# Optimization experiments

Hardware: AMD Instinct MI355X
Metric: run time of the kernel (lower is better)

Reference implementation:

```python
import jax, jax.numpy as jnp
import numpy as np

N_NODES = 50000


def gcn_conv(x, W, b, src, dst, n_nodes):
    """PyG GCNConv: x' = D^-1/2 (A+I) D^-1/2 (x W) + b (symmetric norm, self-loops)."""
    h = x @ W  # [N, out]
    loop = jnp.arange(n_nodes, dtype=src.dtype)
    src_f = jnp.concatenate([src, loop])
    dst_f = jnp.concatenate([dst, loop])
    ones = jnp.ones(src_f.shape[0], dtype=h.dtype)
    deg = jax.ops.segment_sum(ones, dst_f, num_segments=n_nodes)
    dinv = jnp.where(deg > 0, jax.lax.rsqrt(deg), 0.0)
    norm = dinv[src_f] * dinv[dst_f]  # [E+N]
    msg = h[src_f] * norm[:, None]    # irregular gather over edges
    out = jax.ops.segment_sum(msg, dst_f, num_segments=n_nodes)
    return out + b


def setup_inputs() -> dict:
    key = jax.random.key(0)
    ks = jax.random.split(key, 9)
    d_in, d_h = 128, 128
    x = jax.random.normal(ks[0], (N_NODES, d_in), dtype=jnp.float32)
    edge_index = jax.random.randint(ks[1], (2, 800000), 0, N_NODES, dtype=jnp.int64)
    glorot = lambda k, fi, fo: jax.random.normal(k, (fi, fo), dtype=jnp.float32) * jnp.sqrt(2.0 / (fi + fo))
    return {
        "x": x,
        "edge_index": edge_index,
        "W1": glorot(ks[2], d_in, d_h), "b1": jnp.zeros((d_h,), jnp.float32),
        "W2": glorot(ks[3], d_h, d_h), "b2": jnp.zeros((d_h,), jnp.float32),
        "W3": glorot(ks[4], d_h, d_h), "b3": jnp.zeros((d_h,), jnp.float32),
    }


def reference(x, edge_index, W1, b1, W2, b2, W3, b3):
    src, dst = edge_index[0], edge_index[1]
    n = x.shape[0]
    h = jax.nn.relu(gcn_conv(x, W1, b1, src, dst, n))
    h = jax.nn.relu(gcn_conv(h, W2, b2, src, dst, n))
    h = gcn_conv(h, W3, b3, src, dst, n)
    return h
```

## Files before the change

kernel.cpp:

```cpp
#include <hip/hip_runtime.h>

#define N_NODES 50000
#define N_EDGES 800000
#define DIM 128
#define MAXDEG 80
#define EDGE_BLOCKS ((N_EDGES + 255) / 256)
#define WT_BLOCKS 192
#define GEMM_BLOCKS ((N_NODES + 127) / 128)

typedef unsigned int u32;
typedef short bf16x8 __attribute__((ext_vector_type(8)));
typedef float f32x4 __attribute__((ext_vector_type(4)));

static inline size_t alignUp(size_t x) { return (x + 255) & ~size_t(255); }

__device__ inline unsigned short f2bf(float f) {
    union { float f; u32 u; } v; v.f = f;
    u32 r = v.u + 0x7fffu + ((v.u >> 16) & 1u);
    return (unsigned short)(r >> 16);
}
__device__ inline float bf_lo(u32 u) { return __uint_as_float(u << 16); }
__device__ inline float bf_hi(u32 u) { return __uint_as_float(u & 0xffff0000u); }

__global__ __launch_bounds__(256) void prep_kernel(const float* __restrict__ W1,
                                                   const float* __restrict__ W2,
                                                   const float* __restrict__ W3,
                                                   unsigned short* __restrict__ Wt,
                                                   const int* __restrict__ src,
                                                   const int* __restrict__ dst,
                                                   int* __restrict__ cursor,
                                                   int* __restrict__ csr) {
    int bid = blockIdx.x;
    if (bid < WT_BLOCKS) {
        int m = bid >> 6;
        int e = (bid & 63) * 256 + threadIdx.x;
        int n = e >> 7, k = e & 127;
        const float* W = (m == 0) ? W1 : (m == 1) ? W2 : W3;
        Wt[m * DIM * DIM + n * DIM + k] = f2bf(W[(size_t)k * DIM + n]);
        return;
    }
    int i = (bid - WT_BLOCKS) * 256 + threadIdx.x;
    if (i < N_EDGES) {
        int d = dst[i];
        int pos = atomicAdd(&cursor[d], 1);
        if (pos < MAXDEG) csr[d * MAXDEG + pos] = src[i];
    }
}

#define LDSTRIDE 40
__global__ __launch_bounds__(256) void gemm_mfma_kernel(const float* __restrict__ x,
                                                        const unsigned short* __restrict__ Wt,
                                                        unsigned short* __restrict__ hb,
                                                        int n_rows) {
    __shared__ unsigned short As[128 * LDSTRIDE];
    __shared__ unsigned short Bs[128 * LDSTRIDE];
    const int tid = threadIdx.x;
    const int wave = tid >> 6;
    const int lane = tid & 63;
    const int quad = lane >> 4;
    const int l16 = lane & 15;
    const int row0 = blockIdx.x * 128;

    f32x4 acc[2][8];
#pragma unroll
    for (int mt = 0; mt < 2; mt++)
#pragma unroll
        for (int nt = 0; nt < 8; nt++) acc[mt][nt] = (f32x4){0.f, 0.f, 0.f, 0.f};

    for (int k0 = 0; k0 < DIM; k0 += 32) {
#pragma unroll
        for (int p = 0; p < 4; p++) {
            int r = p * 32 + (tid >> 3);
            int kq = (tid & 7) * 4;
            int gr = row0 + r;
            float4 v = make_float4(0.f, 0.f, 0.f, 0.f);
            if (gr < n_rows) v = *(const float4*)&x[(size_t)gr * DIM + k0 + kq];
            u32 lo = (u32)f2bf(v.x) | ((u32)f2bf(v.y) << 16);
            u32 hi = (u32)f2bf(v.z) | ((u32)f2bf(v.w) << 16);
            *(uint2*)&As[r * LDSTRIDE + kq] = make_uint2(lo, hi);
        }
#pragma unroll
        for (int p = 0; p < 2; p++) {
            int nn = p * 64 + (tid >> 2);
            int kk = (tid & 3) * 8;
            *(uint4*)&Bs[nn * LDSTRIDE + kk] = *(const uint4*)&Wt[nn * DIM + k0 + kk];
        }
        __syncthreads();
        const int m0 = wave * 32;
        bf16x8 a0 = *(const bf16x8*)&As[(m0 + l16) * LDSTRIDE + quad * 8];
        bf16x8 a1 = *(const bf16x8*)&As[(m0 + 16 + l16) * LDSTRIDE + quad * 8];
#pragma unroll
        for (int nt = 0; nt < 8; nt++) {
            bf16x8 b = *(const bf16x8*)&Bs[(nt * 16 + l16) * LDSTRIDE + quad * 8];
            acc[0][nt] = __builtin_amdgcn_mfma_f32_16x16x32_bf16(a0, b, acc[0][nt], 0, 0, 0);
            acc[1][nt] = __builtin_amdgcn_mfma_f32_16x16x32_bf16(a1, b, acc[1][nt], 0, 0, 0);
        }
        __syncthreads();
    }
    const int m0 = wave * 32;
#pragma unroll
    for (int mt = 0; mt < 2; mt++) {
#pragma unroll
        for (int reg = 0; reg < 4; reg++) {
            int gr = row0 + m0 + mt * 16 + quad * 4 + reg;
            if (gr < n_rows) {
#pragma unroll
                for (int nt = 0; nt < 8; nt++)
                    hb[(size_t)gr * DIM + nt * 16 + l16] = f2bf(acc[mt][nt][reg]);
            }
        }
    }
}

__device__ inline void accum8(float acc[8], uint4 r, float w) {
    acc[0] += w * bf_lo(r.x); acc[1] += w * bf_hi(r.x);
    acc[2] += w * bf_lo(r.y); acc[3] += w * bf_hi(r.y);
    acc[4] += w * bf_lo(r.z); acc[5] += w * bf_hi(r.z);
    acc[6] += w * bf_lo(r.w); acc[7] += w * bf_hi(r.w);
}

__global__ __launch_bounds__(256) void agg_kernel(const uint4* __restrict__ hb,
                                                  const int* __restrict__ cnt,
                                                  const int* __restrict__ csr,
                                                  const float4* __restrict__ bias4,
                                                  float* __restrict__ out, int relu) {
    const int wave = threadIdx.x >> 6;
    const int lane = threadIdx.x & 63;
    const int node = blockIdx.x * 4 + wave;
    const int g = lane >> 4;
    const int l16 = lane & 15;

    const int deg = cnt[node];
    const float di = rsqrtf((float)(deg + 1));
    const int m_total = min(deg, MAXDEG);
    const size_t start = (size_t)node * MAXDEG;

    float acc[8];
#pragma unroll
    for (int i = 0; i < 8; i++) acc[i] = 0.f;

    for (int base = 0; base < m_total; base += 64) {
        int m = min(64, m_total - base);
        int e = 0; float w = 0.f;
        if (lane < m) {
            e = csr[start + base + lane];
            w = rsqrtf((float)(cnt[e] + 1));
        }
        int j4 = 0;
        for (; j4 + 8 <= m; j4 += 8) {
            int j0 = j4 + g, j1 = j4 + 4 + g;
            int s0 = __shfl(e, j0, 64);  float w0 = __shfl(w, j0, 64);
            int s1 = __shfl(e, j1, 64);  float w1 = __shfl(w, j1, 64);
            uint4 r0 = hb[(size_t)s0 * 16 + l16];
            uint4 r1 = hb[(size_t)s1 * 16 + l16];
            accum8(acc, r0, w0);
            accum8(acc, r1, w1);
        }
        for (; j4 < m; j4 += 4) {
            int j = j4 + g;
            int jj = (j < m) ? j : 0;
            int s0 = __shfl(e, jj, 64);  float w0 = __shfl(w, jj, 64);
            if (j < m) {
                uint4 r0 = hb[(size_t)s0 * 16 + l16];
                accum8(acc, r0, w0);
            }
        }
    }
    if (g == 0) {
        uint4 r = hb[(size_t)node * 16 + l16];
        accum8(acc, r, di);
    }
#pragma unroll
    for (int i = 0; i < 8; i++) {
        acc[i] += __shfl_xor(acc[i], 16, 64);
        acc[i] += __shfl_xor(acc[i], 32, 64);
    }
    if (g == 0) {
        float4 b0 = bias4[l16 * 2], b1 = bias4[l16 * 2 + 1];
        float4 r0 = make_float4(di * acc[0] + b0.x, di * acc[1] + b0.y,
                                di * acc[2] + b0.z, di * acc[3] + b0.w);
        float4 r1 = make_float4(di * acc[4] + b1.x, di * acc[5] + b1.y,
                                di * acc[6] + b1.z, di * acc[7] + b1.w);
        if (relu) {
            r0.x = fmaxf(r0.x, 0.f); r0.y = fmaxf(r0.y, 0.f);
            r0.z = fmaxf(r0.z, 0.f); r0.w = fmaxf(r0.w, 0.f);
            r1.x = fmaxf(r1.x, 0.f); r1.y = fmaxf(r1.y, 0.f);
            r1.z = fmaxf(r1.z, 0.f); r1.w = fmaxf(r1.w, 0.f);
        }
        float4* o = (float4*)(out + (size_t)node * DIM);
        o[l16 * 2] = r0;
        o[l16 * 2 + 1] = r1;
    }
}


extern "C" void kernel_launch(void* const* d_in, const int* in_sizes, int n_in,
                              void* d_out, int out_size, void* d_ws, size_t ws_size,
                              hipStream_t stream) {
    const float* x  = (const float*)d_in[0];
    const int* ei   = (const int*)d_in[1];
    const float* W1 = (const float*)d_in[2];
    const float* b1 = (const float*)d_in[3];
    const float* W2 = (const float*)d_in[4];
    const float* b2 = (const float*)d_in[5];
    const float* W3 = (const float*)d_in[6];
    const float* b3 = (const float*)d_in[7];
    const int* src = ei;
    const int* dst = ei + N_EDGES;
    float* out = (float*)d_out;

    char* w = (char*)d_ws;
    int* cursor = (int*)w; w += alignUp((size_t)N_NODES * 4);
    int* csr    = (int*)w; w += alignUp((size_t)N_NODES * MAXDEG * 4);
    unsigned short* wt = (unsigned short*)w; w += alignUp((size_t)3 * DIM * DIM * 2);
    unsigned short* hbuf = (unsigned short*)w; w += alignUp((size_t)N_NODES * DIM * 2);
    float* fbuf = (float*)w; w += alignUp((size_t)N_NODES * DIM * 4);

    hipMemsetAsync(cursor, 0, (size_t)N_NODES * 4, stream);

    int ablocks = N_NODES / 4;

    prep_kernel<<<WT_BLOCKS + EDGE_BLOCKS, 256, 0, stream>>>(W1, W2, W3, wt, src, dst,
                                                             cursor, csr);

    gemm_mfma_kernel<<<GEMM_BLOCKS, 256, 0, stream>>>(x, wt, hbuf, N_NODES);
    agg_kernel<<<ablocks, 256, 0, stream>>>((const uint4*)hbuf, cursor, csr,
                                            (const float4*)b1, fbuf, 1);

    gemm_mfma_kernel<<<GEMM_BLOCKS, 256, 0, stream>>>(fbuf, wt + DIM * DIM, hbuf, N_NODES);
    agg_kernel<<<ablocks, 256, 0, stream>>>((const uint4*)hbuf, cursor, csr,
                                            (const float4*)b2, fbuf, 1);

    gemm_mfma_kernel<<<GEMM_BLOCKS, 256, 0, stream>>>(fbuf, wt + 2 * DIM * DIM, hbuf, N_NODES);
    agg_kernel<<<ablocks, 256, 0, stream>>>((const uint4*)hbuf, cursor, csr,
                                            (const float4*)b3, out, 0);
}
```

Before: 284.2 us.

## Build compact CSR with prefix-scan offsets, 16-bit indices, precomputed dinv

After: 317.0 us. +11.5%, slower.

```diff
diff --git a/kernel.cpp b/kernel.cpp
--- a/kernel.cpp
+++ b/kernel.cpp
@@ -3,10 +3,10 @@
 #define N_NODES 50000
 #define N_EDGES 800000
 #define DIM 128
-#define MAXDEG 80
 #define EDGE_BLOCKS ((N_EDGES + 255) / 256)
 #define WT_BLOCKS 192
 #define GEMM_BLOCKS ((N_NODES + 127) / 128)
+#define SCAN_BLOCKS ((N_NODES + 255) / 256)
 
 typedef unsigned int u32;
 typedef short bf16x8 __attribute__((ext_vector_type(8)));
@@ -26,10 +26,8 @@
                                                    const float* __restrict__ W2,
                                                    const float* __restrict__ W3,
                                                    unsigned short* __restrict__ Wt,
-                                                   const int* __restrict__ src,
                                                    const int* __restrict__ dst,
-                                                   int* __restrict__ cursor,
-                                                   int* __restrict__ csr) {
+                                                   int* __restrict__ cnt) {
     int bid = blockIdx.x;
     if (bid < WT_BLOCKS) {
         int m = bid >> 6;
@@ -40,10 +38,32 @@
         return;
     }
     int i = (bid - WT_BLOCKS) * 256 + threadIdx.x;
-    if (i < N_EDGES) {
-        int d = dst[i];
-        int pos = atomicAdd(&cursor[d], 1);
-        if (pos < MAXDEG) csr[d * MAXDEG + pos] = src[i];
+    if (i < N_EDGES) atomicAdd(&cnt[dst[i]], 1);
+}
+
+__global__ __launch_bounds__(256) void offsets_kernel(const int* __restrict__ cnt,
+                                                      int* __restrict__ total,
+                                                      int* __restrict__ base,
+                                                      int* __restrict__ cur,
+                                                      float* __restrict__ dinv) {
+    int i = blockIdx.x * 256 + threadIdx.x;
+    int lane = threadIdx.x & 63;
+    int c = (i < N_NODES) ? cnt[i] : 0;
+    int v = c;
+#pragma unroll
+    for (int off = 1; off < 64; off <<= 1) {
+        int u = __shfl_up(v, off, 64);
+        if (lane >= off) v += u;
+    }
+    int wsum = __shfl(v, 63, 64);
+    int wbase = 0;
+    if (lane == 63) wbase = atomicAdd(total, wsum);
+    wbase = __shfl(wbase, 63, 64);
+    if (i < N_NODES) {
+        int b = wbase + v - c;
+        base[i] = b;
+        cur[i]  = b;
+        dinv[i] = rsqrtf((float)(c + 1));
     }
 }
 
@@ -51,7 +71,20 @@
 __global__ __launch_bounds__(256) void gemm_mfma_kernel(const float* __restrict__ x,
                                                         const unsigned short* __restrict__ Wt,
                                                         unsigned short* __restrict__ hb,
-                                                        int n_rows) {
+                                                        int n_rows,
+                                                        const int* __restrict__ src,
+                                                        const int* __restrict__ dst,
+                                                        int* __restrict__ cur,
+                                                        unsigned short* __restrict__ csr16) {
+    if (blockIdx.x >= GEMM_BLOCKS) {
+        int i = (blockIdx.x - GEMM_BLOCKS) * 256 + threadIdx.x;
+        if (i < N_EDGES) {
+            int d = dst[i];
+            int pos = atomicAdd(&cur[d], 1);
+            if (pos < N_EDGES) csr16[pos] = (unsigned short)src[i];
+        }
+        return;
+    }
     __shared__ unsigned short As[128 * LDSTRIDE];
     __shared__ unsigned short Bs[128 * LDSTRIDE];
     const int tid = threadIdx.x;
@@ -121,7 +154,9 @@
 
 __global__ __launch_bounds__(256) void agg_kernel(const uint4* __restrict__ hb,
                                                   const int* __restrict__ cnt,
-                                                  const int* __restrict__ csr,
+                                                  const int* __restrict__ basep,
+                                                  const unsigned short* __restrict__ csr16,
+                                                  const float* __restrict__ dinv,
                                                   const float4* __restrict__ bias4,
                                                   float* __restrict__ out, int relu) {
     const int wave = threadIdx.x >> 6;
@@ -131,20 +166,19 @@
     const int l16 = lane & 15;
 
     const int deg = cnt[node];
-    const float di = rsqrtf((float)(deg + 1));
-    const int m_total = min(deg, MAXDEG);
-    const size_t start = (size_t)node * MAXDEG;
+    const float di = dinv[node];
+    const int start = basep[node];
 
     float acc[8];
 #pragma unroll
     for (int i = 0; i < 8; i++) acc[i] = 0.f;
 
-    for (int base = 0; base < m_total; base += 64) {
-        int m = min(64, m_total - base);
+    for (int b0 = 0; b0 < deg; b0 += 64) {
+        int m = min(64, deg - b0);
         int e = 0; float w = 0.f;
         if (lane < m) {
-            e = csr[start + base + lane];
-            w = rsqrtf((float)(cnt[e] + 1));
+            e = csr16[start + b0 + lane];
+            w = dinv[e];
         }
         int j4 = 0;
         for (; j4 + 8 <= m; j4 += 8) {
@@ -210,28 +244,35 @@
     float* out = (float*)d_out;
 
     char* w = (char*)d_ws;
-    int* cursor = (int*)w; w += alignUp((size_t)N_NODES * 4);
-    int* csr    = (int*)w; w += alignUp((size_t)N_NODES * MAXDEG * 4);
+    int* cnt   = (int*)w; w += alignUp((size_t)(N_NODES + 1) * 4);
+    int* total = cnt + N_NODES;
+    int* base  = (int*)w; w += alignUp((size_t)N_NODES * 4);
+    int* cur   = (int*)w; w += alignUp((size_t)N_NODES * 4);
+    float* dinvb = (float*)w; w += alignUp((size_t)N_NODES * 4);
+    unsigned short* csr16 = (unsigned short*)w; w += alignUp((size_t)N_EDGES * 2);
     unsigned short* wt = (unsigned short*)w; w += alignUp((size_t)3 * DIM * DIM * 2);
     unsigned short* hbuf = (unsigned short*)w; w += alignUp((size_t)N_NODES * DIM * 2);
     float* fbuf = (float*)w; w += alignUp((size_t)N_NODES * DIM * 4);
 
-    hipMemsetAsync(cursor, 0, (size_t)N_NODES * 4, stream);
+    hipMemsetAsync(cnt, 0, (size_t)(N_NODES + 1) * 4, stream);
 
     int ablocks = N_NODES / 4;
 
-    prep_kernel<<<WT_BLOCKS + EDGE_BLOCKS, 256, 0, stream>>>(W1, W2, W3, wt, src, dst,
-                                                             cursor, csr);
-
-    gemm_mfma_kernel<<<GEMM_BLOCKS, 256, 0, stream>>>(x, wt, hbuf, N_NODES);
-    agg_kernel<<<ablocks, 256, 0, stream>>>((const uint4*)hbuf, cursor, csr,
+    prep_kernel<<<WT_BLOCKS + EDGE_BLOCKS, 256, 0, stream>>>(W1, W2, W3, wt, dst, cnt);
+    offsets_kernel<<<SCAN_BLOCKS, 256, 0, stream>>>(cnt, total, base, cur, dinvb);
+
+    gemm_mfma_kernel<<<GEMM_BLOCKS + EDGE_BLOCKS, 256, 0, stream>>>(x, wt, hbuf, N_NODES,
+                                                                    src, dst, cur, csr16);
+    agg_kernel<<<ablocks, 256, 0, stream>>>((const uint4*)hbuf, cnt, base, csr16, dinvb,
                                             (const float4*)b1, fbuf, 1);
 
-    gemm_mfma_kernel<<<GEMM_BLOCKS, 256, 0, stream>>>(fbuf, wt + DIM * DIM, hbuf, N_NODES);
-    agg_kernel<<<ablocks, 256, 0, stream>>>((const uint4*)hbuf, cursor, csr,
+    gemm_mfma_kernel<<<GEMM_BLOCKS, 256, 0, stream>>>(fbuf, wt + DIM * DIM, hbuf, N_NODES,
+                                                      nullptr, nullptr, nullptr, nullptr);
+    agg_kernel<<<ablocks, 256, 0, stream>>>((const uint4*)hbuf, cnt, base, csr16, dinvb,
                                             (const float4*)b2, fbuf, 1);
 
-    gemm_mfma_kernel<<<GEMM_BLOCKS, 256, 0, stream>>>(fbuf, wt + 2 * DIM * DIM, hbuf, N_NODES);
-    agg_kernel<<<ablocks, 256, 0, stream>>>((const uint4*)hbuf, cursor, csr,
+    gemm_mfma_kernel<<<GEMM_BLOCKS, 256, 0, stream>>>(fbuf, wt + 2 * DIM * DIM, hbuf, N_NODES,
+                                                      nullptr, nullptr, nullptr, nullptr);
+    agg_kernel<<<ablocks, 256, 0, stream>>>((const uint4*)hbuf, cnt, base, csr16, dinvb,
                                             (const float4*)b3, out, 0);
 }
```
